# Kernel optimization log

Measured on AMD Instinct MI355X. Metric: run time of the kernel, lower is better.

The kernel has to match this reference:

```python
import jax, jax.numpy as jnp
import numpy as np

B, S, H, F = 256, 196, 1024, 2048  # batch, att_size, hidden/att_hid, att_feat_size


def setup_inputs() -> dict:
    key = jax.random.key(0)
    ks = jax.random.split(key, 10)
    sc = 1.0 / np.sqrt(H)
    return {
        "ha": jax.random.normal(ks[0], (B, H), jnp.float32),
        "hf": jax.random.normal(ks[1], (B, H), jnp.float32),
        "att_feats": jax.random.normal(ks[2], (B, S, F), jnp.float32),
        "p_att_feats": jax.random.normal(ks[3], (B, S, H), jnp.float32),
        "W_ha": jax.random.normal(ks[4], (H, H), jnp.float32) * sc,
        "b_ha": jax.random.normal(ks[5], (H,), jnp.float32) * sc,
        "W_hf": jax.random.normal(ks[6], (H, H), jnp.float32) * sc,
        "b_hf": jax.random.normal(ks[7], (H,), jnp.float32) * sc,
        "w_alpha": jax.random.normal(ks[8], (H,), jnp.float32) * sc,
        "b_alpha": jax.random.normal(ks[9], (1,), jnp.float32) * sc,
    }


def reference(ha, hf, att_feats, p_att_feats, W_ha, b_ha, W_hf, b_hf, w_alpha, b_alpha):
    # additive (Bahdanau-style) attention with two query projections
    att_ha = ha @ W_ha.T + b_ha          # [B, H]
    att_hf = hf @ W_hf.T + b_hf          # [B, H]
    dot = jnp.tanh(att_ha[:, None, :] + att_hf[:, None, :] + p_att_feats)  # [B, S, H]
    scores = jnp.einsum("bsh,h->bs", dot, w_alpha) + b_alpha[0]            # [B, S]
    weight = jax.nn.softmax(scores, axis=1)                                 # [B, S]
    att_res = jnp.einsum("bs,bsf->bf", weight, att_feats)                   # [B, F]
    return att_res
```

## Files before the change

### kernel.cpp

```cpp
#include <hip/hip_runtime.h>
#include <hip/hip_bf16.h>

#define Bdim 256
#define Sdim 196
#define Hdim 1024
#define Fdim 2048
#define BH (Bdim*Hdim)
#define L2E 1.44269504f
#define C2L 2.88539008f

typedef float nfloat4 __attribute__((ext_vector_type(4)));

__device__ __forceinline__ float4 ldnt4(const float* p) {
    nfloat4 v = __builtin_nontemporal_load(reinterpret_cast<const nfloat4*>(p));
    return make_float4(v.x, v.y, v.z, v.w);
}

#define TM 64
#define TN 128
#define TK 32

__global__ __launch_bounds__(256) void gemm_q_part(
    const float* __restrict__ ha, const float* __restrict__ hf,
    const float* __restrict__ Wha, const float* __restrict__ Whf,
    float* __restrict__ qpart, int kchunk)
{
    __shared__ float As[TK][TM + 4];
    __shared__ float Ws[TK][TN + 4];

    const int tid = threadIdx.x;
    const int th  = tid & 15;
    const int tb  = tid >> 4;
    const int h0  = blockIdx.x * TN;
    const int b0  = blockIdx.y * TM;
    const int z   = blockIdx.z;
    const int kv_base = z * kchunk;

    float acc[4][8];
    #pragma unroll
    for (int i = 0; i < 4; ++i)
        #pragma unroll
        for (int j = 0; j < 8; ++j) acc[i][j] = 0.0f;

    float4 xv[2], wv[4];

    auto load_regs = [&](int t) {
        int kv = kv_base + t * TK;
        const float* X; const float* W; int k0;
        if (kv < 1024) { X = ha; W = Wha; k0 = kv; }
        else           { X = hf; W = Whf; k0 = kv - 1024; }
        #pragma unroll
        for (int r = 0; r < 2; ++r) {
            int idx = tid + r * 256;
            int row = idx >> 3, kq = idx & 7;
            xv[r] = *reinterpret_cast<const float4*>(X + (size_t)(b0 + row) * Hdim + k0 + kq * 4);
        }
        #pragma unroll
        for (int r = 0; r < 4; ++r) {
            int idx = tid + r * 256;
            int row = idx >> 3, kq = idx & 7;
            wv[r] = *reinterpret_cast<const float4*>(W + (size_t)(h0 + row) * Hdim + k0 + kq * 4);
        }
    };

    const int ntiles = kchunk / TK;
    load_regs(0);

    for (int t = 0; t < ntiles; ++t) {
        #pragma unroll
        for (int r = 0; r < 2; ++r) {
            int idx = tid + r * 256;
            int row = idx >> 3, kq = idx & 7;
            As[kq * 4 + 0][row] = xv[r].x;
            As[kq * 4 + 1][row] = xv[r].y;
            As[kq * 4 + 2][row] = xv[r].z;
            As[kq * 4 + 3][row] = xv[r].w;
        }
        #pragma unroll
        for (int r = 0; r < 4; ++r) {
            int idx = tid + r * 256;
            int row = idx >> 3, kq = idx & 7;
            Ws[kq * 4 + 0][row] = wv[r].x;
            Ws[kq * 4 + 1][row] = wv[r].y;
            Ws[kq * 4 + 2][row] = wv[r].z;
            Ws[kq * 4 + 3][row] = wv[r].w;
        }
        __syncthreads();

        if (t + 1 < ntiles) load_regs(t + 1);

        #pragma unroll
        for (int k = 0; k < TK; ++k) {
            float4 a0 = *reinterpret_cast<const float4*>(&As[k][tb * 4]);
            float4 w0 = *reinterpret_cast<const float4*>(&Ws[k][th * 8]);
            float4 w1 = *reinterpret_cast<const float4*>(&Ws[k][th * 8 + 4]);
            float a[4] = {a0.x, a0.y, a0.z, a0.w};
            float w[8] = {w0.x, w0.y, w0.z, w0.w, w1.x, w1.y, w1.z, w1.w};
            #pragma unroll
            for (int i = 0; i < 4; ++i)
                #pragma unroll
                for (int j = 0; j < 8; ++j)
                    acc[i][j] += a[i] * w[j];
        }
        __syncthreads();
    }

    #pragma unroll
    for (int i = 0; i < 4; ++i) {
        int b = b0 + tb * 4 + i;
        float* dst = qpart + (size_t)z * BH + (size_t)b * Hdim + h0 + th * 8;
        float4 o0 = {acc[i][0], acc[i][1], acc[i][2], acc[i][3]};
        float4 o1 = {acc[i][4], acc[i][5], acc[i][6], acc[i][7]};
        *reinterpret_cast<float4*>(dst)     = o0;
        *reinterpret_cast<float4*>(dst + 4) = o1;
    }
}

__global__ __launch_bounds__(1024) void fused_kernel(
    const float* __restrict__ qpart, const float* __restrict__ b_ha,
    const float* __restrict__ b_hf,  const float* __restrict__ p_att,
    const float* __restrict__ w_alpha, const float* __restrict__ b_alpha,
    const float* __restrict__ att_feats, float* __restrict__ out, int ks)
{
    __shared__ __align__(16) float qs2[Hdim];
    __shared__ __align__(16) float wa_s[Hdim];
    __shared__ __align__(16) float sc[Sdim];
    __shared__ __align__(16) float part[Fdim];
    __shared__ __align__(16) float qtmp[3 * Hdim];
    __shared__ float wred[5];

    const int b    = blockIdx.x;
    const int tid  = threadIdx.x;
    const int wave = tid >> 6, lane = tid & 63;

    {
        const int zg = tid >> 8;
        const int h4 = tid & 255;
        size_t off = (size_t)b * Hdim + h4 * 4;
        float4 s = {0.f, 0.f, 0.f, 0.f};
        for (int z = zg; z < ks; z += 4) {
            float4 v = *reinterpret_cast<const float4*>(qpart + (size_t)z * BH + off);
            s.x += v.x; s.y += v.y; s.z += v.z; s.w += v.w;
        }
        if (zg > 0) {
            *reinterpret_cast<float4*>(qtmp + (zg - 1) * Hdim + h4 * 4) = s;
        } else {
            float4 ba = *reinterpret_cast<const float4*>(b_ha + h4 * 4);
            float4 bb = *reinterpret_cast<const float4*>(b_hf + h4 * 4);
            s.x += ba.x + bb.x; s.y += ba.y + bb.y;
            s.z += ba.z + bb.z; s.w += ba.w + bb.w;
            *reinterpret_cast<float4*>(qs2 + h4 * 4) = s;
        }
        if (zg == 1) {
            float4 w = *reinterpret_cast<const float4*>(w_alpha + h4 * 4);
            *reinterpret_cast<float4*>(wa_s + h4 * 4) = w;
            float ls = w.x + w.y + w.z + w.w;
            #pragma unroll
            for (int m = 32; m >= 1; m >>= 1) ls += __shfl_xor(ls, m, 64);
            if (lane == 0) wred[wave - 4] = ls;
        }
    }
    __syncthreads();

    if (tid < 256) {
        const int h4 = tid;
        float4 s = *reinterpret_cast<const float4*>(qs2 + h4 * 4);
        #pragma unroll
        for (int g = 0; g < 3; ++g) {
            float4 v = *reinterpret_cast<const float4*>(qtmp + g * Hdim + h4 * 4);
            s.x += v.x; s.y += v.y; s.z += v.z; s.w += v.w;
        }
        s.x *= C2L; s.y *= C2L; s.z *= C2L; s.w *= C2L;
        *reinterpret_cast<float4*>(qs2 + h4 * 4) = s;
    }
    __syncthreads();

    const float base_sc = wred[0] + wred[1] + wred[2] + wred[3] + b_alpha[0];

    float4 qr[4], wr[4];
    #pragma unroll
    for (int i = 0; i < 4; ++i) {
        qr[i] = *reinterpret_cast<const float4*>(qs2 + (i * 64 + lane) * 4);
        wr[i] = *reinterpret_cast<const float4*>(wa_s + (i * 64 + lane) * 4);
    }

    const float* pbase = p_att + (size_t)b * Sdim * Hdim;
    {
        int s = wave;
        float4 pv[4];
        #pragma unroll
        for (int i = 0; i < 4; ++i)
            pv[i] = ldnt4(pbase + (size_t)s * Hdim + (i * 64 + lane) * 4);
        while (s < Sdim) {
            const int sn = s + 16;
            float4 pn[4];
            if (sn < Sdim) {
                #pragma unroll
                for (int i = 0; i < 4; ++i)
                    pn[i] = ldnt4(pbase + (size_t)sn * Hdim + (i * 64 + lane) * 4);
            }
            float psum = 0.0f;
            #pragma unroll
            for (int i = 0; i < 4; ++i) {
                psum += wr[i].x * __builtin_amdgcn_rcpf(__builtin_amdgcn_exp2f(fmaf(pv[i].x, C2L, qr[i].x)) + 1.0f);
                psum += wr[i].y * __builtin_amdgcn_rcpf(__builtin_amdgcn_exp2f(fmaf(pv[i].y, C2L, qr[i].y)) + 1.0f);
                psum += wr[i].z * __builtin_amdgcn_rcpf(__builtin_amdgcn_exp2f(fmaf(pv[i].z, C2L, qr[i].z)) + 1.0f);
                psum += wr[i].w * __builtin_amdgcn_rcpf(__builtin_amdgcn_exp2f(fmaf(pv[i].w, C2L, qr[i].w)) + 1.0f);
            }
            #pragma unroll
            for (int m = 32; m >= 1; m >>= 1) psum += __shfl_xor(psum, m, 64);
            if (lane == 0) sc[s] = base_sc - 2.0f * psum;
            #pragma unroll
            for (int i = 0; i < 4; ++i) pv[i] = pn[i];
            s = sn;
        }
    }
    __syncthreads();

    if (wave == 0) {
        float v0 = sc[lane];
        float v1 = sc[lane + 64];
        float v2 = sc[lane + 128];
        float v3 = (lane < Sdim - 192) ? sc[lane + 192] : -1e30f;
        float m = fmaxf(fmaxf(v0, v1), fmaxf(v2, v3));
        #pragma unroll
        for (int mk = 32; mk >= 1; mk >>= 1) m = fmaxf(m, __shfl_xor(m, mk, 64));
        float e0 = __builtin_amdgcn_exp2f((v0 - m) * L2E);
        float e1 = __builtin_amdgcn_exp2f((v1 - m) * L2E);
        float e2 = __builtin_amdgcn_exp2f((v2 - m) * L2E);
        float e3 = (lane < Sdim - 192) ? __builtin_amdgcn_exp2f((v3 - m) * L2E) : 0.0f;
        float ss = e0 + e1 + e2 + e3;
        #pragma unroll
        for (int mk = 32; mk >= 1; mk >>= 1) ss += __shfl_xor(ss, mk, 64);
        sc[lane]       = e0;
        sc[lane + 64]  = e1;
        sc[lane + 128] = e2;
        if (lane < Sdim - 192) sc[lane + 192] = e3;
        if (lane == 0) wred[4] = __builtin_amdgcn_rcpf(ss);
    }
    __syncthreads();

    const int half = tid >> 9;
    const int fi   = (tid & 511) * 4;
    const float* abase = att_feats + (size_t)b * Sdim * Fdim + fi;
    float4 a4 = {0.f, 0.f, 0.f, 0.f};
    const int s0 = half ? 96 : 0;
    const int s1 = half ? 196 : 96;
    for (int s4 = s0; s4 < s1; s4 += 4) {
        float4 w4 = *reinterpret_cast<const float4*>(sc + s4);
        float4 v0 = ldnt4(abase + (size_t)(s4 + 0) * Fdim);
        float4 v1 = ldnt4(abase + (size_t)(s4 + 1) * Fdim);
        float4 v2 = ldnt4(abase + (size_t)(s4 + 2) * Fdim);
        float4 v3 = ldnt4(abase + (size_t)(s4 + 3) * Fdim);
        a4.x += w4.x * v0.x; a4.y += w4.x * v0.y; a4.z += w4.x * v0.z; a4.w += w4.x * v0.w;
        a4.x += w4.y * v1.x; a4.y += w4.y * v1.y; a4.z += w4.y * v1.z; a4.w += w4.y * v1.w;
        a4.x += w4.z * v2.x; a4.y += w4.z * v2.y; a4.z += w4.z * v2.z; a4.w += w4.z * v2.w;
        a4.x += w4.w * v3.x; a4.y += w4.w * v3.y; a4.z += w4.w * v3.z; a4.w += w4.w * v3.w;
    }
    if (half) {
        *reinterpret_cast<float4*>(part + fi) = a4;
    }
    __syncthreads();
    if (!half) {
        const float winv = wred[4];
        float4 p4 = *reinterpret_cast<const float4*>(part + fi);
        a4.x = (a4.x + p4.x) * winv; a4.y = (a4.y + p4.y) * winv;
        a4.z = (a4.z + p4.z) * winv; a4.w = (a4.w + p4.w) * winv;
        *reinterpret_cast<float4*>(out + (size_t)b * Fdim + fi) = a4;
    }
}

extern "C" void kernel_launch(void* const* d_in, const int* in_sizes, int n_in,
                              void* d_out, int out_size, void* d_ws, size_t ws_size,
                              hipStream_t stream) {
    const float* ha       = (const float*)d_in[0];
    const float* hf       = (const float*)d_in[1];
    const float* att_f    = (const float*)d_in[2];
    const float* p_att    = (const float*)d_in[3];
    const float* W_ha     = (const float*)d_in[4];
    const float* b_ha     = (const float*)d_in[5];
    const float* W_hf     = (const float*)d_in[6];
    const float* b_hf     = (const float*)d_in[7];
    const float* w_alpha  = (const float*)d_in[8];
    const float* b_alpha  = (const float*)d_in[9];
    float* out = (float*)d_out;
    float* ws  = (float*)d_ws;

    int KS = 16;
    while (KS > 1 && ((size_t)KS * BH) * sizeof(float) > ws_size) KS >>= 1;

    float* qpart = ws;

    dim3 gA(Hdim / TN, Bdim / TM, KS);
    gemm_q_part<<<gA, 256, 0, stream>>>(ha, hf, W_ha, W_hf, qpart, 2048 / KS);

    fused_kernel<<<dim3(Bdim), 1024, 0, stream>>>(
        qpart, b_ha, b_hf, p_att, w_alpha, b_alpha, att_f, out, KS);
}
```

Baseline: 122.2 us.

## Store split-K partials in fp16, enlarge GEMM tile, fuse softmax exp into weighted sum

The split-K query GEMM tile grows from 64x128 to 128x128, so each thread accumulates 8x8 outputs, and the partial sums are written to the workspace as fp16 instead of fp32, halving partial-sum traffic. The fused kernel now has every wave compute the softmax max and sum redundantly, which removes a barrier and the write-back of exponentials. The exponentials are then computed inline in the att_feats reduction loop, now unrolled by 8. The fp16 partials lose precision in the attention query, and the larger GEMM tile halves the block count and raises register pressure.

```diff
diff --git a/kernel.cpp b/kernel.cpp
--- a/kernel.cpp
+++ b/kernel.cpp
@@ -1,5 +1,6 @@
 #include <hip/hip_runtime.h>
 #include <hip/hip_bf16.h>
+#include <hip/hip_fp16.h>
 
 #define Bdim 256
 #define Sdim 196
@@ -16,14 +17,14 @@
     return make_float4(v.x, v.y, v.z, v.w);
 }
 
-#define TM 64
+#define TM 128
 #define TN 128
 #define TK 32
 
 __global__ __launch_bounds__(256) void gemm_q_part(
     const float* __restrict__ ha, const float* __restrict__ hf,
     const float* __restrict__ Wha, const float* __restrict__ Whf,
-    float* __restrict__ qpart, int kchunk)
+    __half* __restrict__ qpart, int kchunk)
 {
     __shared__ float As[TK][TM + 4];
     __shared__ float Ws[TK][TN + 4];
@@ -36,13 +37,13 @@
     const int z   = blockIdx.z;
     const int kv_base = z * kchunk;
 
-    float acc[4][8];
+    float acc[8][8];
     #pragma unroll
-    for (int i = 0; i < 4; ++i)
+    for (int i = 0; i < 8; ++i)
         #pragma unroll
         for (int j = 0; j < 8; ++j) acc[i][j] = 0.0f;
 
-    float4 xv[2], wv[4];
+    float4 xv[4], wv[4];
 
     auto load_regs = [&](int t) {
         int kv = kv_base + t * TK;
@@ -50,15 +51,10 @@
         if (kv < 1024) { X = ha; W = Wha; k0 = kv; }
         else           { X = hf; W = Whf; k0 = kv - 1024; }
         #pragma unroll
-        for (int r = 0; r < 2; ++r) {
+        for (int r = 0; r < 4; ++r) {
             int idx = tid + r * 256;
             int row = idx >> 3, kq = idx & 7;
             xv[r] = *reinterpret_cast<const float4*>(X + (size_t)(b0 + row) * Hdim + k0 + kq * 4);
-        }
-        #pragma unroll
-        for (int r = 0; r < 4; ++r) {
-            int idx = tid + r * 256;
-            int row = idx >> 3, kq = idx & 7;
             wv[r] = *reinterpret_cast<const float4*>(W + (size_t)(h0 + row) * Hdim + k0 + kq * 4);
         }
     };
@@ -68,18 +64,13 @@
 
     for (int t = 0; t < ntiles; ++t) {
         #pragma unroll
-        for (int r = 0; r < 2; ++r) {
+        for (int r = 0; r < 4; ++r) {
             int idx = tid + r * 256;
             int row = idx >> 3, kq = idx & 7;
             As[kq * 4 + 0][row] = xv[r].x;
             As[kq * 4 + 1][row] = xv[r].y;
             As[kq * 4 + 2][row] = xv[r].z;
             As[kq * 4 + 3][row] = xv[r].w;
-        }
-        #pragma unroll
-        for (int r = 0; r < 4; ++r) {
-            int idx = tid + r * 256;
-            int row = idx >> 3, kq = idx & 7;
             Ws[kq * 4 + 0][row] = wv[r].x;
             Ws[kq * 4 + 1][row] = wv[r].y;
             Ws[kq * 4 + 2][row] = wv[r].z;
@@ -91,13 +82,14 @@
 
         #pragma unroll
         for (int k = 0; k < TK; ++k) {
-            float4 a0 = *reinterpret_cast<const float4*>(&As[k][tb * 4]);
+            float4 a0 = *reinterpret_cast<const float4*>(&As[k][tb * 8]);
+            float4 a1 = *reinterpret_cast<const float4*>(&As[k][tb * 8 + 4]);
             float4 w0 = *reinterpret_cast<const float4*>(&Ws[k][th * 8]);
             float4 w1 = *reinterpret_cast<const float4*>(&Ws[k][th * 8 + 4]);
-            float a[4] = {a0.x, a0.y, a0.z, a0.w};
+            float a[8] = {a0.x, a0.y, a0.z, a0.w, a1.x, a1.y, a1.z, a1.w};
             float w[8] = {w0.x, w0.y, w0.z, w0.w, w1.x, w1.y, w1.z, w1.w};
             #pragma unroll
-            for (int i = 0; i < 4; ++i)
+            for (int i = 0; i < 8; ++i)
                 #pragma unroll
                 for (int j = 0; j < 8; ++j)
                     acc[i][j] += a[i] * w[j];
@@ -106,18 +98,19 @@
     }
 
     #pragma unroll
-    for (int i = 0; i < 4; ++i) {
-        int b = b0 + tb * 4 + i;
-        float* dst = qpart + (size_t)z * BH + (size_t)b * Hdim + h0 + th * 8;
-        float4 o0 = {acc[i][0], acc[i][1], acc[i][2], acc[i][3]};
-        float4 o1 = {acc[i][4], acc[i][5], acc[i][6], acc[i][7]};
-        *reinterpret_cast<float4*>(dst)     = o0;
-        *reinterpret_cast<float4*>(dst + 4) = o1;
+    for (int i = 0; i < 8; ++i) {
+        int b = b0 + tb * 8 + i;
+        __half* dst = qpart + (size_t)z * BH + (size_t)b * Hdim + h0 + th * 8;
+        __half2* dst2 = reinterpret_cast<__half2*>(dst);
+        dst2[0] = __floats2half2_rn(acc[i][0], acc[i][1]);
+        dst2[1] = __floats2half2_rn(acc[i][2], acc[i][3]);
+        dst2[2] = __floats2half2_rn(acc[i][4], acc[i][5]);
+        dst2[3] = __floats2half2_rn(acc[i][6], acc[i][7]);
     }
 }
 
 __global__ __launch_bounds__(1024) void fused_kernel(
-    const float* __restrict__ qpart, const float* __restrict__ b_ha,
+    const __half* __restrict__ qpart, const float* __restrict__ b_ha,
     const float* __restrict__ b_hf,  const float* __restrict__ p_att,
     const float* __restrict__ w_alpha, const float* __restrict__ b_alpha,
     const float* __restrict__ att_feats, float* __restrict__ out, int ks)
@@ -127,7 +120,7 @@
     __shared__ __align__(16) float sc[Sdim];
     __shared__ __align__(16) float part[Fdim];
     __shared__ __align__(16) float qtmp[3 * Hdim];
-    __shared__ float wred[5];
+    __shared__ float wred[4];
 
     const int b    = blockIdx.x;
     const int tid  = threadIdx.x;
@@ -139,8 +132,10 @@
         size_t off = (size_t)b * Hdim + h4 * 4;
         float4 s = {0.f, 0.f, 0.f, 0.f};
         for (int z = zg; z < ks; z += 4) {
-            float4 v = *reinterpret_cast<const float4*>(qpart + (size_t)z * BH + off);
-            s.x += v.x; s.y += v.y; s.z += v.z; s.w += v.w;
+            const __half2* p2 = reinterpret_cast<const __half2*>(qpart + (size_t)z * BH + off);
+            float2 f0 = __half22float2(p2[0]);
+            float2 f1 = __half22float2(p2[1]);
+            s.x += f0.x; s.y += f0.y; s.z += f1.x; s.w += f1.y;
         }
         if (zg > 0) {
             *reinterpret_cast<float4*>(qtmp + (zg - 1) * Hdim + h4 * 4) = s;
@@ -217,7 +212,8 @@
     }
     __syncthreads();
 
-    if (wave == 0) {
+    float m_max, ssum;
+    {
         float v0 = sc[lane];
         float v1 = sc[lane + 64];
         float v2 = sc[lane + 128];
@@ -232,13 +228,8 @@
         float ss = e0 + e1 + e2 + e3;
         #pragma unroll
         for (int mk = 32; mk >= 1; mk >>= 1) ss += __shfl_xor(ss, mk, 64);
-        sc[lane]       = e0;
-        sc[lane + 64]  = e1;
-        sc[lane + 128] = e2;
-        if (lane < Sdim - 192) sc[lane + 192] = e3;
-        if (lane == 0) wred[4] = __builtin_amdgcn_rcpf(ss);
-    }
-    __syncthreads();
+        m_max = m; ssum = ss;
+    }
 
     const int half = tid >> 9;
     const int fi   = (tid & 511) * 4;
@@ -246,23 +237,56 @@
     float4 a4 = {0.f, 0.f, 0.f, 0.f};
     const int s0 = half ? 96 : 0;
     const int s1 = half ? 196 : 96;
-    for (int s4 = s0; s4 < s1; s4 += 4) {
-        float4 w4 = *reinterpret_cast<const float4*>(sc + s4);
+    int s4 = s0;
+    for (; s4 + 8 <= s1; s4 += 8) {
+        float4 sa = *reinterpret_cast<const float4*>(sc + s4);
+        float4 sb = *reinterpret_cast<const float4*>(sc + s4 + 4);
         float4 v0 = ldnt4(abase + (size_t)(s4 + 0) * Fdim);
         float4 v1 = ldnt4(abase + (size_t)(s4 + 1) * Fdim);
         float4 v2 = ldnt4(abase + (size_t)(s4 + 2) * Fdim);
         float4 v3 = ldnt4(abase + (size_t)(s4 + 3) * Fdim);
-        a4.x += w4.x * v0.x; a4.y += w4.x * v0.y; a4.z += w4.x * v0.z; a4.w += w4.x * v0.w;
-        a4.x += w4.y * v1.x; a4.y += w4.y * v1.y; a4.z += w4.y * v1.z; a4.w += w4.y * v1.w;
-        a4.x += w4.z * v2.x; a4.y += w4.z * v2.y; a4.z += w4.z * v2.z; a4.w += w4.z * v2.w;
-        a4.x += w4.w * v3.x; a4.y += w4.w * v3.y; a4.z += w4.w * v3.z; a4.w += w4.w * v3.w;
+        float4 v4 = ldnt4(abase + (size_t)(s4 + 4) * Fdim);
+        float4 v5 = ldnt4(abase + (size_t)(s4 + 5) * Fdim);
+        float4 v6 = ldnt4(abase + (size_t)(s4 + 6) * Fdim);
+        float4 v7 = ldnt4(abase + (size_t)(s4 + 7) * Fdim);
+        float e0 = __builtin_amdgcn_exp2f((sa.x - m_max) * L2E);
+        float e1 = __builtin_amdgcn_exp2f((sa.y - m_max) * L2E);
+        float e2 = __builtin_amdgcn_exp2f((sa.z - m_max) * L2E);
+        float e3 = __builtin_amdgcn_exp2f((sa.w - m_max) * L2E);
+        float e4 = __builtin_amdgcn_exp2f((sb.x - m_max) * L2E);
+        float e5 = __builtin_amdgcn_exp2f((sb.y - m_max) * L2E);
+        float e6 = __builtin_amdgcn_exp2f((sb.z - m_max) * L2E);
+        float e7 = __builtin_amdgcn_exp2f((sb.w - m_max) * L2E);
+        a4.x += e0 * v0.x; a4.y += e0 * v0.y; a4.z += e0 * v0.z; a4.w += e0 * v0.w;
+        a4.x += e1 * v1.x; a4.y += e1 * v1.y; a4.z += e1 * v1.z; a4.w += e1 * v1.w;
+        a4.x += e2 * v2.x; a4.y += e2 * v2.y; a4.z += e2 * v2.z; a4.w += e2 * v2.w;
+        a4.x += e3 * v3.x; a4.y += e3 * v3.y; a4.z += e3 * v3.z; a4.w += e3 * v3.w;
+        a4.x += e4 * v4.x; a4.y += e4 * v4.y; a4.z += e4 * v4.z; a4.w += e4 * v4.w;
+        a4.x += e5 * v5.x; a4.y += e5 * v5.y; a4.z += e5 * v5.z; a4.w += e5 * v5.w;
+        a4.x += e6 * v6.x; a4.y += e6 * v6.y; a4.z += e6 * v6.z; a4.w += e6 * v6.w;
+        a4.x += e7 * v7.x; a4.y += e7 * v7.y; a4.z += e7 * v7.z; a4.w += e7 * v7.w;
+    }
+    if (s4 < s1) {
+        float4 sa = *reinterpret_cast<const float4*>(sc + s4);
+        float4 v0 = ldnt4(abase + (size_t)(s4 + 0) * Fdim);
+        float4 v1 = ldnt4(abase + (size_t)(s4 + 1) * Fdim);
+        float4 v2 = ldnt4(abase + (size_t)(s4 + 2) * Fdim);
+        float4 v3 = ldnt4(abase + (size_t)(s4 + 3) * Fdim);
+        float e0 = __builtin_amdgcn_exp2f((sa.x - m_max) * L2E);
+        float e1 = __builtin_amdgcn_exp2f((sa.y - m_max) * L2E);
+        float e2 = __builtin_amdgcn_exp2f((sa.z - m_max) * L2E);
+        float e3 = __builtin_amdgcn_exp2f((sa.w - m_max) * L2E);
+        a4.x += e0 * v0.x; a4.y += e0 * v0.y; a4.z += e0 * v0.z; a4.w += e0 * v0.w;
+        a4.x += e1 * v1.x; a4.y += e1 * v1.y; a4.z += e1 * v1.z; a4.w += e1 * v1.w;
+        a4.x += e2 * v2.x; a4.y += e2 * v2.y; a4.z += e2 * v2.z; a4.w += e2 * v2.w;
+        a4.x += e3 * v3.x; a4.y += e3 * v3.y; a4.z += e3 * v3.z; a4.w += e3 * v3.w;
     }
     if (half) {
         *reinterpret_cast<float4*>(part + fi) = a4;
     }
     __syncthreads();
     if (!half) {
-        const float winv = wred[4];
+        const float winv = __builtin_amdgcn_rcpf(ssum);
         float4 p4 = *reinterpret_cast<const float4*>(part + fi);
         a4.x = (a4.x + p4.x) * winv; a4.y = (a4.y + p4.y) * winv;
         a4.z = (a4.z + p4.z) * winv; a4.w = (a4.w + p4.w) * winv;
@@ -284,12 +308,10 @@
     const float* w_alpha  = (const float*)d_in[8];
     const float* b_alpha  = (const float*)d_in[9];
     float* out = (float*)d_out;
-    float* ws  = (float*)d_ws;
+    __half* qpart = (__half*)d_ws;
 
     int KS = 16;
-    while (KS > 1 && ((size_t)KS * BH) * sizeof(float) > ws_size) KS >>= 1;
-
-    float* qpart = ws;
+    while (KS > 1 && ((size_t)KS * BH) * sizeof(__half) > ws_size) KS >>= 1;
 
     dim3 gA(Hdim / TN, Bdim / TM, KS);
     gemm_q_part<<<gA, 256, 0, stream>>>(ha, hf, W_ha, W_hf, qpart, 2048 / KS);
```

New measurement: 120.5 us. No clear change (-1.4%).
